# Kernel optimization log

Measured on AMD Instinct MI355X. Metric: run time of the kernel, lower is better.

## Reference

```python
import jax, jax.numpy as jnp
import numpy as np

B, S, D_IN, D_OUT = 4, 2048, 1024, 1024

def setup_inputs() -> dict:
    key = jax.random.key(0)
    k1, k2, k3, k4 = jax.random.split(key, 4)
    x = jax.random.normal(k1, (B, S, D_IN), dtype=jnp.float32)
    # torch Linear weight is [d_out, d_in]; store as [d_in, d_out] for x @ W
    scale = 1.0 / np.sqrt(D_IN)
    Wq = jax.random.normal(k2, (D_IN, D_OUT), dtype=jnp.float32) * scale
    Wk = jax.random.normal(k3, (D_IN, D_OUT), dtype=jnp.float32) * scale
    Wv = jax.random.normal(k4, (D_IN, D_OUT), dtype=jnp.float32) * scale
    return {"x": x, "Wq": Wq, "Wk": Wk, "Wv": Wv}

def reference(x, Wq, Wk, Wv):
    b, n, _ = x.shape
    q = jnp.einsum('bnd,de->bne', x, Wq)
    k = jnp.einsum('bnd,de->bne', x, Wk)
    v = jnp.einsum('bnd,de->bne', x, Wv)
    scores = jnp.einsum('bqe,bke->bqk', q, k) / jnp.sqrt(jnp.float32(k.shape[-1]))
    causal = jnp.tril(jnp.ones((n, n), dtype=bool))  # True = keep
    scores = jnp.where(causal[None], scores, -jnp.inf)
    attn = jax.nn.softmax(scores, axis=-1)
    # dropout p=0.0 -> identity (eval-equivalent)
    return jnp.einsum('bqk,bke->bqe', attn, v)
```

## Files before the change

### kernel.cpp

```cpp
#include <hip/hip_runtime.h>
#include <hip/hip_bf16.h>
#include <math.h>

typedef __hip_bfloat16 bf16;
typedef __attribute__((ext_vector_type(8))) short short8;
typedef __attribute__((ext_vector_type(4))) float f32x4;

#define GLD16(gp, lp)                                                          \
    __builtin_amdgcn_global_load_lds(                                          \
        (const __attribute__((address_space(1))) unsigned int*)(gp),           \
        (__attribute__((address_space(3))) unsigned int*)(lp), 16, 0, 0)


__global__ __launch_bounds__(256) void cvt_x(const float* __restrict__ in,
                                             bf16* __restrict__ out) {
    long base = ((long)blockIdx.x * 256 + threadIdx.x) * 8;
    const float4* p = (const float4*)(in + base);
    float4 a = p[0], b = p[1];
    union { bf16 h[8]; short8 v; } o;
    o.h[0] = __float2bfloat16(a.x); o.h[1] = __float2bfloat16(a.y);
    o.h[2] = __float2bfloat16(a.z); o.h[3] = __float2bfloat16(a.w);
    o.h[4] = __float2bfloat16(b.x); o.h[5] = __float2bfloat16(b.y);
    o.h[6] = __float2bfloat16(b.z); o.h[7] = __float2bfloat16(b.w);
    *(short8*)(out + base) = o.v;
}

__global__ __launch_bounds__(256) void cvt_w_t(const float* __restrict__ Wq,
                                               const float* __restrict__ Wk,
                                               const float* __restrict__ Wv,
                                               bf16* __restrict__ WT) {
    const float* W = blockIdx.z == 0 ? Wq : (blockIdx.z == 1 ? Wk : Wv);
    bf16* T = WT + (long)blockIdx.z * 1024 * 1024;
    __shared__ float t[32][33];
    int n0 = blockIdx.x * 32, k0 = blockIdx.y * 32;
    int tx = threadIdx.x, ty = threadIdx.y;
    #pragma unroll
    for (int i = 0; i < 4; ++i)
        t[ty * 4 + i][tx] = W[(long)(k0 + ty * 4 + i) * 1024 + n0 + tx];
    __syncthreads();
    #pragma unroll
    for (int i = 0; i < 4; ++i)
        T[(long)(n0 + ty * 4 + i) * 1024 + k0 + tx] =
            __float2bfloat16(t[tx][ty * 4 + i]);
}

template <int MODE, bool TRI, bool PVK>
__global__ __launch_bounds__(256) void gemm_bt(
    const bf16* __restrict__ A, const bf16* __restrict__ B,
    void* __restrict__ C0, void* __restrict__ C1, void* __restrict__ C2,
    float* __restrict__ RS, int K, int lda, int ldb, int ldc, float alpha,
    long az, long bz, long cz) {
    int tm, tn, bi = 0;
    if (MODE == 1) {
        tn = blockIdx.x; tm = blockIdx.y;
    } else if (TRI) {
        int t = blockIdx.x % 136;
        bi = blockIdx.x / 136;
        int i = (int)((sqrtf(8.f * t + 1.f) - 1.f) * 0.5f);
        while ((i + 1) * (i + 2) / 2 <= t) ++i;
        while (i * (i + 1) / 2 > t) --i;
        tm = i; tn = t - i * (i + 1) / 2;
    } else {
        tm = 15 - (int)(blockIdx.x >> 5);
        int r = blockIdx.x & 31;
        tn = r & 7; bi = r >> 3;
    }
    const int Keff = PVK ? (tm + 1) * 128 : K;
    A += (long)bi * az;
    B += (long)bi * bz;

    const int m0 = tm * 128, n0 = tn * 128;
    __shared__ bf16 As[2][128 * 32];
    __shared__ bf16 Bs[2][128 * 32];

    const int tid = threadIdx.x;
    const int wave = tid >> 6, lane = tid & 63;
    const int wr = wave >> 1, wc = wave & 1;
    const int lrow = lane & 15, kg = lane >> 4;

    f32x4 acc[4][4];
    #pragma unroll
    for (int i = 0; i < 4; ++i)
        #pragma unroll
        for (int j = 0; j < 4; ++j) acc[i][j] = (f32x4){0.f, 0.f, 0.f, 0.f};

    const int srow = tid >> 2;
    const int scol = ((((srow >> 1) & 3) ^ (tid & 3)) << 3);
    const bf16* ap = A + (long)(m0 + srow) * lda + scol;
    const bf16* bp = B + (long)(n0 + srow) * ldb + scol;
    const int nk = Keff >> 5;

    {
        char* ad = (char*)(&As[0][0]) + tid * 16;
        char* bd = (char*)(&Bs[0][0]) + tid * 16;
        GLD16(ap, ad);
        GLD16(ap + 64L * lda, ad + 4096);
        GLD16(bp, bd);
        GLD16(bp + 64L * ldb, bd + 4096);
    }
    __syncthreads();

    for (int t = 0; t < nk; ++t) {
        const int cur = t & 1;
        if (t + 1 < nk) {
            const int k0 = (t + 1) << 5;
            char* ad = (char*)(&As[cur ^ 1][0]) + tid * 16;
            char* bd = (char*)(&Bs[cur ^ 1][0]) + tid * 16;
            GLD16(ap + k0, ad);
            GLD16(ap + 64L * lda + k0, ad + 4096);
            GLD16(bp + k0, bd);
            GLD16(bp + 64L * ldb + k0, bd + 4096);
        }
        short8 af[4], bfr[4];
        #pragma unroll
        for (int mi = 0; mi < 4; ++mi) {
            const int ck = ((mi * 8 + (lrow >> 1)) & 3) ^ kg;
            af[mi] = *(const short8*)(&As[cur][(wr * 64 + mi * 16 + lrow) * 32 + ck * 8]);
        }
        #pragma unroll
        for (int ni = 0; ni < 4; ++ni) {
            const int ck = ((ni * 8 + (lrow >> 1)) & 3) ^ kg;
            bfr[ni] = *(const short8*)(&Bs[cur][(wc * 64 + ni * 16 + lrow) * 32 + ck * 8]);
        }
        #pragma unroll
        for (int mi = 0; mi < 4; ++mi)
            #pragma unroll
            for (int ni = 0; ni < 4; ++ni)
                acc[mi][ni] = __builtin_amdgcn_mfma_f32_16x16x32_bf16(
                    af[mi], bfr[ni], acc[mi][ni], 0, 0, 0);
        __syncthreads();
    }

    const int rb = wr * 64 + (lane >> 4) * 4;
    const int cb = wc * 64 + (lane & 15);
    if (MODE == 0) {
        bf16* E = (bf16*)C0 + (long)bi * cz;
        float* rsb = RS + bi * 2048;
        #pragma unroll
        for (int mi = 0; mi < 4; ++mi)
            #pragma unroll
            for (int j = 0; j < 4; ++j) {
                const int gq = m0 + rb + mi * 16 + j;
                float rp = 0.f;
                #pragma unroll
                for (int ni = 0; ni < 4; ++ni) {
                    const int gk = n0 + cb + ni * 16;
                    float e = (gk <= gq) ? __expf(acc[mi][ni][j] * alpha) : 0.f;
                    E[(long)gq * 2048 + gk] = __float2bfloat16(e);
                    rp += e;
                }
                #pragma unroll
                for (int o = 1; o < 16; o <<= 1) rp += __shfl_xor(rp, o);
                if ((lane & 15) == 0) atomicAdd(rsb + gq, rp);
            }
    } else if (MODE == 2) {
        float* Cf = (float*)C0 + (long)bi * cz;
        const float* rsb = RS + bi * 2048;
        #pragma unroll
        for (int mi = 0; mi < 4; ++mi)
            #pragma unroll
            for (int j = 0; j < 4; ++j) {
                const int gq = m0 + rb + mi * 16 + j;
                const float inv = 1.f / rsb[gq];
                #pragma unroll
                for (int ni = 0; ni < 4; ++ni)
                    Cf[(long)gq * ldc + (n0 + cb + ni * 16)] =
                        acc[mi][ni][j] * inv;
            }
    } else {
        const int sel = n0 >> 10;
        const int nb = n0 & 1023;
        if (sel < 2) {
            bf16* Cb = sel ? (bf16*)C1 : (bf16*)C0;
            #pragma unroll
            for (int mi = 0; mi < 4; ++mi)
                #pragma unroll
                for (int ni = 0; ni < 4; ++ni)
                    #pragma unroll
                    for (int j = 0; j < 4; ++j)
                        Cb[(long)(m0 + rb + mi * 16 + j) * 1024 + (nb + cb + ni * 16)] =
                            __float2bfloat16(acc[mi][ni][j]);
        } else {
            bf16* T = (bf16*)C2;
            #pragma unroll
            for (int mi = 0; mi < 4; ++mi)
                #pragma unroll
                for (int ni = 0; ni < 4; ++ni) {
                    int gm = m0 + rb + mi * 16;
                    int col = nb + cb + ni * 16;
                    int b = gm >> 11, mm = gm & 2047;
                    union { bf16 h[4]; ushort4 v; } o;
                    #pragma unroll
                    for (int j = 0; j < 4; ++j)
                        o.h[j] = __float2bfloat16(acc[mi][ni][j]);
                    *(ushort4*)(T + (long)b * 2097152 + (long)col * 2048 + mm) = o.v;
                }
        }
    }
}

extern "C" void kernel_launch(void* const* d_in, const int* in_sizes, int n_in,
                              void* d_out, int out_size, void* d_ws,
                              size_t ws_size, hipStream_t stream) {
    const float* x = (const float*)d_in[0];
    const float* Wq = (const float*)d_in[1];
    const float* Wk = (const float*)d_in[2];
    const float* Wv = (const float*)d_in[3];
    float* out = (float*)d_out;

    char* ws = (char*)d_ws;
    bf16* xb = (bf16*)ws;
    bf16* wt = (bf16*)(ws + 16777216);
    bf16* Qb = (bf16*)(ws + 23068672);
    bf16* Kb = (bf16*)(ws + 39845888);
    bf16* VT = (bf16*)(ws + 56623104);
    bf16* E  = (bf16*)(ws + 73400320);
    float* rs = (float*)(ws + 106954752);
    if (ws_size < 106987520) return;

    cvt_x<<<4096, 256, 0, stream>>>(x, xb);
    cvt_w_t<<<dim3(32, 32, 3), dim3(32, 8), 0, stream>>>(Wq, Wk, Wv, wt);
    hipMemsetAsync(rs, 0, 4 * 2048 * sizeof(float), stream);
    gemm_bt<1, false, false><<<dim3(24, 64), 256, 0, stream>>>(
        xb, wt, Qb, Kb, VT, nullptr, 1024, 1024, 1024, 0, 1.f, 0, 0, 0);
    gemm_bt<0, true, false><<<544, 256, 0, stream>>>(
        Qb, Kb, E, nullptr, nullptr, rs, 1024, 1024, 1024, 2048, 0.03125f,
        2097152, 2097152, 4194304);
    gemm_bt<2, false, true><<<512, 256, 0, stream>>>(
        E, VT, out, nullptr, nullptr, rs, 2048, 2048, 2048, 1024, 1.f,
        4194304, 2097152, 2097152);
}
```

Measured before the change: 246.3 us.

## Split GEMMs into specialized kernels with 64-row attention tiles and single-buffered LDS

Replaces the templated gemm_bt with a dedicated QKV projection kernel and an attention GEMM kernel. The attention kernels now use 64x128 tiles with a 64-row triangular mapping, which doubles the block count and trims wasted work on the causal diagonal. All kernels also drop LDS double buffering in favour of a load-sync-compute-sync loop. This lowers LDS use and may raise occupancy, but global loads no longer overlap with MFMA work inside a block.

After: 243.5 us. About the same (-1.1%).

```diff
diff --git a/kernel.cpp b/kernel.cpp
--- a/kernel.cpp
+++ b/kernel.cpp
@@ -44,34 +44,13 @@
             __float2bfloat16(t[tx][ty * 4 + i]);
 }
 
-template <int MODE, bool TRI, bool PVK>
-__global__ __launch_bounds__(256) void gemm_bt(
+__global__ __launch_bounds__(256) void gemm_qkv(
     const bf16* __restrict__ A, const bf16* __restrict__ B,
-    void* __restrict__ C0, void* __restrict__ C1, void* __restrict__ C2,
-    float* __restrict__ RS, int K, int lda, int ldb, int ldc, float alpha,
-    long az, long bz, long cz) {
-    int tm, tn, bi = 0;
-    if (MODE == 1) {
-        tn = blockIdx.x; tm = blockIdx.y;
-    } else if (TRI) {
-        int t = blockIdx.x % 136;
-        bi = blockIdx.x / 136;
-        int i = (int)((sqrtf(8.f * t + 1.f) - 1.f) * 0.5f);
-        while ((i + 1) * (i + 2) / 2 <= t) ++i;
-        while (i * (i + 1) / 2 > t) --i;
-        tm = i; tn = t - i * (i + 1) / 2;
-    } else {
-        tm = 15 - (int)(blockIdx.x >> 5);
-        int r = blockIdx.x & 31;
-        tn = r & 7; bi = r >> 3;
-    }
-    const int Keff = PVK ? (tm + 1) * 128 : K;
-    A += (long)bi * az;
-    B += (long)bi * bz;
-
+    bf16* __restrict__ Q, bf16* __restrict__ Kd, bf16* __restrict__ VT) {
+    const int tn = blockIdx.x, tm = blockIdx.y;
     const int m0 = tm * 128, n0 = tn * 128;
-    __shared__ bf16 As[2][128 * 32];
-    __shared__ bf16 Bs[2][128 * 32];
+    __shared__ bf16 As[128 * 32];
+    __shared__ bf16 Bs[128 * 32];
 
     const int tid = threadIdx.x;
     const int wave = tid >> 6, lane = tid & 63;
@@ -86,41 +65,27 @@
 
     const int srow = tid >> 2;
     const int scol = ((((srow >> 1) & 3) ^ (tid & 3)) << 3);
-    const bf16* ap = A + (long)(m0 + srow) * lda + scol;
-    const bf16* bp = B + (long)(n0 + srow) * ldb + scol;
-    const int nk = Keff >> 5;
-
-    {
-        char* ad = (char*)(&As[0][0]) + tid * 16;
-        char* bd = (char*)(&Bs[0][0]) + tid * 16;
-        GLD16(ap, ad);
-        GLD16(ap + 64L * lda, ad + 4096);
-        GLD16(bp, bd);
-        GLD16(bp + 64L * ldb, bd + 4096);
-    }
-    __syncthreads();
-
-    for (int t = 0; t < nk; ++t) {
-        const int cur = t & 1;
-        if (t + 1 < nk) {
-            const int k0 = (t + 1) << 5;
-            char* ad = (char*)(&As[cur ^ 1][0]) + tid * 16;
-            char* bd = (char*)(&Bs[cur ^ 1][0]) + tid * 16;
-            GLD16(ap + k0, ad);
-            GLD16(ap + 64L * lda + k0, ad + 4096);
-            GLD16(bp + k0, bd);
-            GLD16(bp + 64L * ldb + k0, bd + 4096);
-        }
+    const bf16* ap = A + (long)(m0 + srow) * 1024 + scol;
+    const bf16* bp = B + (long)(n0 + srow) * 1024 + scol;
+    char* asb = (char*)As + tid * 16;
+    char* bsb = (char*)Bs + tid * 16;
+
+    for (int k0 = 0; k0 < 1024; k0 += 32) {
+        GLD16(ap + k0, asb);
+        GLD16(ap + 64L * 1024 + k0, asb + 4096);
+        GLD16(bp + k0, bsb);
+        GLD16(bp + 64L * 1024 + k0, bsb + 4096);
+        __syncthreads();
         short8 af[4], bfr[4];
         #pragma unroll
         for (int mi = 0; mi < 4; ++mi) {
-            const int ck = ((mi * 8 + (lrow >> 1)) & 3) ^ kg;
-            af[mi] = *(const short8*)(&As[cur][(wr * 64 + mi * 16 + lrow) * 32 + ck * 8]);
+            const int rr = wr * 64 + mi * 16 + lrow;
+            af[mi] = *(const short8*)(&As[rr * 32 + ((((rr >> 1) & 3) ^ kg) << 3)]);
         }
         #pragma unroll
         for (int ni = 0; ni < 4; ++ni) {
-            const int ck = ((ni * 8 + (lrow >> 1)) & 3) ^ kg;
-            bfr[ni] = *(const short8*)(&Bs[cur][(wc * 64 + ni * 16 + lrow) * 32 + ck * 8]);
+            const int rr = wc * 64 + ni * 16 + lrow;
+            bfr[ni] = *(const short8*)(&Bs[rr * 32 + ((((rr >> 1) & 3) ^ kg) << 3)]);
         }
         #pragma unroll
         for (int mi = 0; mi < 4; ++mi)
@@ -133,11 +98,114 @@
 
     const int rb = wr * 64 + (lane >> 4) * 4;
     const int cb = wc * 64 + (lane & 15);
+    const int sel = n0 >> 10;
+    const int nb = n0 & 1023;
+    if (sel < 2) {
+        bf16* Cb = sel ? Kd : Q;
+        #pragma unroll
+        for (int mi = 0; mi < 4; ++mi)
+            #pragma unroll
+            for (int ni = 0; ni < 4; ++ni)
+                #pragma unroll
+                for (int j = 0; j < 4; ++j)
+                    Cb[(long)(m0 + rb + mi * 16 + j) * 1024 + (nb + cb + ni * 16)] =
+                        __float2bfloat16(acc[mi][ni][j]);
+    } else {
+        #pragma unroll
+        for (int mi = 0; mi < 4; ++mi)
+            #pragma unroll
+            for (int ni = 0; ni < 4; ++ni) {
+                int gm = m0 + rb + mi * 16;
+                int col = nb + cb + ni * 16;
+                int b = gm >> 11, mm = gm & 2047;
+                union { bf16 h[4]; ushort4 v; } o;
+                #pragma unroll
+                for (int j = 0; j < 4; ++j)
+                    o.h[j] = __float2bfloat16(acc[mi][ni][j]);
+                *(ushort4*)(VT + (long)b * 2097152 + (long)col * 2048 + mm) = o.v;
+            }
+    }
+}
+
+template <int MODE>
+__global__ __launch_bounds__(256) void gemm_att(
+    const bf16* __restrict__ A, const bf16* __restrict__ B,
+    void* __restrict__ C, float* __restrict__ RS, int lda, int ldb,
+    float alpha, long az, long bz) {
+    int tm, tn, bi;
     if (MODE == 0) {
-        bf16* E = (bf16*)C0 + (long)bi * cz;
+        int t = blockIdx.x % 272;
+        bi = blockIdx.x / 272;
+        int m = 2 * (int)sqrtf((float)t);
+        if (m > 31) m = 31;
+        auto cum = [](int mm) { int u = mm >> 1; return (mm & 1) ? (u + 1) * (u + 1) : u * u + u; };
+        while (m < 31 && cum(m + 1) <= t) ++m;
+        while (cum(m) > t) --m;
+        tm = m; tn = t - cum(m);
+    } else {
+        tm = 31 - (int)(blockIdx.x >> 5);
+        int r = blockIdx.x & 31;
+        tn = r & 7; bi = r >> 3;
+    }
+    const int nk = (MODE == 0) ? 32 : 2 * (tm + 1);
+    A += (long)bi * az;
+    B += (long)bi * bz;
+
+    const int m0 = tm * 64, n0 = tn * 128;
+    __shared__ bf16 As[64 * 32];
+    __shared__ bf16 Bs[128 * 32];
+
+    const int tid = threadIdx.x;
+    const int wave = tid >> 6, lane = tid & 63;
+    const int wr2 = wave >> 1, wc2 = wave & 1;
+    const int lrow = lane & 15, kg = lane >> 4;
+
+    f32x4 acc[2][4];
+    #pragma unroll
+    for (int i = 0; i < 2; ++i)
+        #pragma unroll
+        for (int j = 0; j < 4; ++j) acc[i][j] = (f32x4){0.f, 0.f, 0.f, 0.f};
+
+    const int srow = tid >> 2;
+    const int scol = ((((srow >> 1) & 3) ^ (tid & 3)) << 3);
+    const bf16* ap = A + (long)(m0 + srow) * lda + scol;
+    const bf16* bp = B + (long)(n0 + srow) * ldb + scol;
+    char* asb = (char*)As + tid * 16;
+    char* bsb = (char*)Bs + tid * 16;
+
+    for (int t = 0; t < nk; ++t) {
+        const int k0 = t << 5;
+        GLD16(ap + k0, asb);
+        GLD16(bp + k0, bsb);
+        GLD16(bp + 64L * ldb + k0, bsb + 4096);
+        __syncthreads();
+        short8 af[2], bfr[4];
+        #pragma unroll
+        for (int mi = 0; mi < 2; ++mi) {
+            const int rr = wr2 * 32 + mi * 16 + lrow;
+            af[mi] = *(const short8*)(&As[rr * 32 + ((((rr >> 1) & 3) ^ kg) << 3)]);
+        }
+        #pragma unroll
+        for (int ni = 0; ni < 4; ++ni) {
+            const int rr = wc2 * 64 + ni * 16 + lrow;
+            bfr[ni] = *(const short8*)(&Bs[rr * 32 + ((((rr >> 1) & 3) ^ kg) << 3)]);
+        }
+        #pragma unroll
+        for (int mi = 0; mi < 2; ++mi)
+            #pragma unroll
+            for (int ni = 0; ni < 4; ++ni)
+                acc[mi][ni] = __builtin_amdgcn_mfma_f32_16x16x32_bf16(
+                    af[mi], bfr[ni], acc[mi][ni], 0, 0, 0);
+        __syncthreads();
+    }
+
+    const int rb = wr2 * 32 + (lane >> 4) * 4;
+    const int cb = wc2 * 64 + (lane & 15);
+    if (MODE == 0) {
+        bf16* E = (bf16*)C + (long)bi * 4194304;
         float* rsb = RS + bi * 2048;
         #pragma unroll
-        for (int mi = 0; mi < 4; ++mi)
+        for (int mi = 0; mi < 2; ++mi)
             #pragma unroll
             for (int j = 0; j < 4; ++j) {
                 const int gq = m0 + rb + mi * 16 + j;
@@ -153,49 +221,20 @@
                 for (int o = 1; o < 16; o <<= 1) rp += __shfl_xor(rp, o);
                 if ((lane & 15) == 0) atomicAdd(rsb + gq, rp);
             }
-    } else if (MODE == 2) {
-        float* Cf = (float*)C0 + (long)bi * cz;
+    } else {
+        float* Cf = (float*)C + (long)bi * 2097152;
         const float* rsb = RS + bi * 2048;
         #pragma unroll
-        for (int mi = 0; mi < 4; ++mi)
+        for (int mi = 0; mi < 2; ++mi)
             #pragma unroll
             for (int j = 0; j < 4; ++j) {
                 const int gq = m0 + rb + mi * 16 + j;
                 const float inv = 1.f / rsb[gq];
                 #pragma unroll
                 for (int ni = 0; ni < 4; ++ni)
-                    Cf[(long)gq * ldc + (n0 + cb + ni * 16)] =
+                    Cf[(long)gq * 1024 + (n0 + cb + ni * 16)] =
                         acc[mi][ni][j] * inv;
             }
-    } else {
-        const int sel = n0 >> 10;
-        const int nb = n0 & 1023;
-        if (sel < 2) {
-            bf16* Cb = sel ? (bf16*)C1 : (bf16*)C0;
-            #pragma unroll
-            for (int mi = 0; mi < 4; ++mi)
-                #pragma unroll
-                for (int ni = 0; ni < 4; ++ni)
-                    #pragma unroll
-                    for (int j = 0; j < 4; ++j)
-                        Cb[(long)(m0 + rb + mi * 16 + j) * 1024 + (nb + cb + ni * 16)] =
-                            __float2bfloat16(acc[mi][ni][j]);
-        } else {
-            bf16* T = (bf16*)C2;
-            #pragma unroll
-            for (int mi = 0; mi < 4; ++mi)
-                #pragma unroll
-                for (int ni = 0; ni < 4; ++ni) {
-                    int gm = m0 + rb + mi * 16;
-                    int col = nb + cb + ni * 16;
-                    int b = gm >> 11, mm = gm & 2047;
-                    union { bf16 h[4]; ushort4 v; } o;
-                    #pragma unroll
-                    for (int j = 0; j < 4; ++j)
-                        o.h[j] = __float2bfloat16(acc[mi][ni][j]);
-                    *(ushort4*)(T + (long)b * 2097152 + (long)col * 2048 + mm) = o.v;
-                }
-        }
     }
 }
 
@@ -221,12 +260,9 @@
     cvt_x<<<4096, 256, 0, stream>>>(x, xb);
     cvt_w_t<<<dim3(32, 32, 3), dim3(32, 8), 0, stream>>>(Wq, Wk, Wv, wt);
     hipMemsetAsync(rs, 0, 4 * 2048 * sizeof(float), stream);
-    gemm_bt<1, false, false><<<dim3(24, 64), 256, 0, stream>>>(
-        xb, wt, Qb, Kb, VT, nullptr, 1024, 1024, 1024, 0, 1.f, 0, 0, 0);
-    gemm_bt<0, true, false><<<544, 256, 0, stream>>>(
-        Qb, Kb, E, nullptr, nullptr, rs, 1024, 1024, 1024, 2048, 0.03125f,
-        2097152, 2097152, 4194304);
-    gemm_bt<2, false, true><<<512, 256, 0, stream>>>(
-        E, VT, out, nullptr, nullptr, rs, 2048, 2048, 2048, 1024, 1.f,
-        4194304, 2097152, 2097152);
-}
+    gemm_qkv<<<dim3(24, 64), 256, 0, stream>>>(xb, wt, Qb, Kb, VT);
+    gemm_att<0><<<1088, 256, 0, stream>>>(
+        Qb, Kb, E, rs, 1024, 1024, 0.03125f, 2097152, 2097152);
+    gemm_att<2><<<1024, 256, 0, stream>>>(
+        E, VT, out, rs, 2048, 2048, 1.f, 4194304, 2097152);
+}
```

## Switch GEMM to single-buffered BK=64 tiles with 8-way XOR swizzle

Applied to the files above, without the earlier changes.

Replaces the double-buffered BK=32 LDS pipeline with a single-buffered BK=64 tile. Each iteration loads the whole tile, syncs, runs two MFMA sub-steps, then syncs again. The change halves the number of k-iterations and barriers and keeps LDS use the same (32 KB). In exchange it gives up overlap between global loads and compute within a block, relying on multiple resident blocks to hide latency. It also hardcodes the strides and K trip counts.

Measured after the change: 251.1 us. About the same (+2.0%).

```diff
diff --git a/kernel.cpp b/kernel.cpp
--- a/kernel.cpp
+++ b/kernel.cpp
@@ -44,16 +44,15 @@
             __float2bfloat16(t[tx][ty * 4 + i]);
 }
 
-template <int MODE, bool TRI, bool PVK>
+template <int MODE>
 __global__ __launch_bounds__(256) void gemm_bt(
     const bf16* __restrict__ A, const bf16* __restrict__ B,
     void* __restrict__ C0, void* __restrict__ C1, void* __restrict__ C2,
-    float* __restrict__ RS, int K, int lda, int ldb, int ldc, float alpha,
-    long az, long bz, long cz) {
+    float* __restrict__ RS, int lda, int ldb, float alpha, long az, long bz) {
     int tm, tn, bi = 0;
     if (MODE == 1) {
         tn = blockIdx.x; tm = blockIdx.y;
-    } else if (TRI) {
+    } else if (MODE == 0) {
         int t = blockIdx.x % 136;
         bi = blockIdx.x / 136;
         int i = (int)((sqrtf(8.f * t + 1.f) - 1.f) * 0.5f);
@@ -65,13 +64,13 @@
         int r = blockIdx.x & 31;
         tn = r & 7; bi = r >> 3;
     }
-    const int Keff = PVK ? (tm + 1) * 128 : K;
+    const int nk = (MODE == 2) ? 2 * (tm + 1) : 16;
     A += (long)bi * az;
     B += (long)bi * bz;
 
     const int m0 = tm * 128, n0 = tn * 128;
-    __shared__ bf16 As[2][128 * 32];
-    __shared__ bf16 Bs[2][128 * 32];
+    __shared__ bf16 As[128 * 64];
+    __shared__ bf16 Bs[128 * 64];
 
     const int tid = threadIdx.x;
     const int wave = tid >> 6, lane = tid & 63;
@@ -84,57 +83,53 @@
         #pragma unroll
         for (int j = 0; j < 4; ++j) acc[i][j] = (f32x4){0.f, 0.f, 0.f, 0.f};
 
-    const int srow = tid >> 2;
-    const int scol = ((((srow >> 1) & 3) ^ (tid & 3)) << 3);
+    const int srow = tid >> 3;
+    const int scol = (((tid & 7) ^ (srow & 7)) << 3);
     const bf16* ap = A + (long)(m0 + srow) * lda + scol;
     const bf16* bp = B + (long)(n0 + srow) * ldb + scol;
-    const int nk = Keff >> 5;
-
-    {
-        char* ad = (char*)(&As[0][0]) + tid * 16;
-        char* bd = (char*)(&Bs[0][0]) + tid * 16;
-        GLD16(ap, ad);
-        GLD16(ap + 64L * lda, ad + 4096);
-        GLD16(bp, bd);
-        GLD16(bp + 64L * ldb, bd + 4096);
-    }
-    __syncthreads();
+    char* asb = (char*)As + tid * 16;
+    char* bsb = (char*)Bs + tid * 16;
 
     for (int t = 0; t < nk; ++t) {
-        const int cur = t & 1;
-        if (t + 1 < nk) {
-            const int k0 = (t + 1) << 5;
-            char* ad = (char*)(&As[cur ^ 1][0]) + tid * 16;
-            char* bd = (char*)(&Bs[cur ^ 1][0]) + tid * 16;
-            GLD16(ap + k0, ad);
-            GLD16(ap + 64L * lda + k0, ad + 4096);
-            GLD16(bp + k0, bd);
-            GLD16(bp + 64L * ldb + k0, bd + 4096);
+        const int k0 = t << 6;
+        GLD16(ap + k0, asb);
+        GLD16(ap + 32L * lda + k0, asb + 4096);
+        GLD16(ap + 64L * lda + k0, asb + 8192);
+        GLD16(ap + 96L * lda + k0, asb + 12288);
+        GLD16(bp + k0, bsb);
+        GLD16(bp + 32L * ldb + k0, bsb + 4096);
+        GLD16(bp + 64L * ldb + k0, bsb + 8192);
+        GLD16(bp + 96L * ldb + k0, bsb + 12288);
+        __syncthreads();
+        #pragma unroll
+        for (int kk = 0; kk < 2; ++kk) {
+            short8 af[4], bfr[4];
+            #pragma unroll
+            for (int mi = 0; mi < 4; ++mi) {
+                const int rr = wr * 64 + mi * 16 + lrow;
+                const int ch = ((kk << 2) | kg) ^ (rr & 7);
+                af[mi] = *(const short8*)(&As[rr * 64 + (ch << 3)]);
+            }
+            #pragma unroll
+            for (int ni = 0; ni < 4; ++ni) {
+                const int rr = wc * 64 + ni * 16 + lrow;
+                const int ch = ((kk << 2) | kg) ^ (rr & 7);
+                bfr[ni] = *(const short8*)(&Bs[rr * 64 + (ch << 3)]);
+            }
+            #pragma unroll
+            for (int mi = 0; mi < 4; ++mi)
+                #pragma unroll
+                for (int ni = 0; ni < 4; ++ni)
+                    acc[mi][ni] = __builtin_amdgcn_mfma_f32_16x16x32_bf16(
+                        af[mi], bfr[ni], acc[mi][ni], 0, 0, 0);
         }
-        short8 af[4], bfr[4];
-        #pragma unroll
-        for (int mi = 0; mi < 4; ++mi) {
-            const int ck = ((mi * 8 + (lrow >> 1)) & 3) ^ kg;
-            af[mi] = *(const short8*)(&As[cur][(wr * 64 + mi * 16 + lrow) * 32 + ck * 8]);
-        }
-        #pragma unroll
-        for (int ni = 0; ni < 4; ++ni) {
-            const int ck = ((ni * 8 + (lrow >> 1)) & 3) ^ kg;
-            bfr[ni] = *(const short8*)(&Bs[cur][(wc * 64 + ni * 16 + lrow) * 32 + ck * 8]);
-        }
-        #pragma unroll
-        for (int mi = 0; mi < 4; ++mi)
-            #pragma unroll
-            for (int ni = 0; ni < 4; ++ni)
-                acc[mi][ni] = __builtin_amdgcn_mfma_f32_16x16x32_bf16(
-                    af[mi], bfr[ni], acc[mi][ni], 0, 0, 0);
         __syncthreads();
     }
 
     const int rb = wr * 64 + (lane >> 4) * 4;
     const int cb = wc * 64 + (lane & 15);
     if (MODE == 0) {
-        bf16* E = (bf16*)C0 + (long)bi * cz;
+        bf16* E = (bf16*)C0 + (long)bi * 4194304;
         float* rsb = RS + bi * 2048;
         #pragma unroll
         for (int mi = 0; mi < 4; ++mi)
@@ -154,7 +149,7 @@
                 if ((lane & 15) == 0) atomicAdd(rsb + gq, rp);
             }
     } else if (MODE == 2) {
-        float* Cf = (float*)C0 + (long)bi * cz;
+        float* Cf = (float*)C0 + (long)bi * 2097152;
         const float* rsb = RS + bi * 2048;
         #pragma unroll
         for (int mi = 0; mi < 4; ++mi)
@@ -164,7 +159,7 @@
                 const float inv = 1.f / rsb[gq];
                 #pragma unroll
                 for (int ni = 0; ni < 4; ++ni)
-                    Cf[(long)gq * ldc + (n0 + cb + ni * 16)] =
+                    Cf[(long)gq * 1024 + (n0 + cb + ni * 16)] =
                         acc[mi][ni][j] * inv;
             }
     } else {
@@ -221,12 +216,11 @@
     cvt_x<<<4096, 256, 0, stream>>>(x, xb);
     cvt_w_t<<<dim3(32, 32, 3), dim3(32, 8), 0, stream>>>(Wq, Wk, Wv, wt);
     hipMemsetAsync(rs, 0, 4 * 2048 * sizeof(float), stream);
-    gemm_bt<1, false, false><<<dim3(24, 64), 256, 0, stream>>>(
-        xb, wt, Qb, Kb, VT, nullptr, 1024, 1024, 1024, 0, 1.f, 0, 0, 0);
-    gemm_bt<0, true, false><<<544, 256, 0, stream>>>(
-        Qb, Kb, E, nullptr, nullptr, rs, 1024, 1024, 1024, 2048, 0.03125f,
-        2097152, 2097152, 4194304);
-    gemm_bt<2, false, true><<<512, 256, 0, stream>>>(
-        E, VT, out, nullptr, nullptr, rs, 2048, 2048, 2048, 1024, 1.f,
-        4194304, 2097152, 2097152);
-}
+    gemm_bt<1><<<dim3(24, 64), 256, 0, stream>>>(
+        xb, wt, Qb, Kb, VT, nullptr, 1024, 1024, 1.f, 0, 0);
+    gemm_bt<0><<<544, 256, 0, stream>>>(
+        Qb, Kb, E, nullptr, nullptr, rs, 1024, 1024, 0.03125f, 2097152,
+        2097152);
+    gemm_bt<2><<<512, 256, 0, stream>>>(
+        E, VT, out, nullptr, nullptr, rs, 2048, 2048, 1.f, 4194304, 2097152);
+}
```
